# Kernel tuning notes

Hardware: AMD Instinct MI355X
Metric: run time of the kernel (lower is better)

The kernel has to match this reference:

```python
import jax, jax.numpy as jnp
import numpy as np

B, P, H, W = 64, 2, 512, 512

def setup_inputs() -> dict:
    key = jax.random.key(0)
    k1, k2 = jax.random.split(key)
    inp = jax.random.normal(k1, (B, P, H, W), dtype=jnp.float32)
    tgt = jax.random.uniform(k2, (B, P, H, W), dtype=jnp.float32)
    return {"input": inp, "target": tgt}


def reference(input, target):
    b, p, h, w = input.shape  # p == 2 required by the original loss
    # DSNT soft-argmax: softmax over flattened heatmap, expectation over grids
    sm = jax.nn.softmax(input.reshape(b, p, h * w), axis=-1).reshape(b, p, h, w)
    x_grid = (jnp.arange(1, w + 1, dtype=input.dtype)) / w  # [W]
    y_grid = (jnp.arange(1, h + 1, dtype=input.dtype)) / h  # [H]
    pred_x = jnp.einsum('bphw,w->bp', sm, x_grid)
    pred_y = jnp.einsum('bphw,h->bp', sm, y_grid)
    # ground-truth argmax coords (detached / non-differentiable)
    am = jnp.argmax(target.reshape(b, p, h * w), axis=-1)  # [B,P]
    true_x = ((am % w).astype(input.dtype) + 1.0) / w
    true_y = ((am // w).astype(input.dtype) + 1.0) / h
    # euclidean distance loss per (sample, point)
    ed = jnp.sqrt((true_x - pred_x) ** 2 + (true_y - pred_y) ** 2)  # [B,P]
    s = jnp.sum(ed)
    # vector between point 0 and point 1 (x, y) per sample
    pred_vec = jnp.stack([pred_x[:, 0] - pred_x[:, 1], pred_y[:, 0] - pred_y[:, 1]], axis=-1)  # [B,2]
    true_vec = jnp.stack([true_x[:, 0] - true_x[:, 1], true_y[:, 0] - true_y[:, 1]], axis=-1)  # [B,2]
    pred_dist = jnp.sqrt(jnp.sum(pred_vec ** 2, axis=-1))  # [B]
    true_dist = jnp.sqrt(jnp.sum(true_vec ** 2, axis=-1))  # [B]
    s = s + jnp.sum(jnp.sqrt((pred_dist - true_dist) ** 2))
    # NOTE: original applies cos() to the cosine similarity (faithful reproduction)
    dot = jnp.sum(pred_vec * true_vec, axis=-1)  # [B]
    cos_distance = 1.0 - jnp.cos(dot / (pred_dist * true_dist))
    s = s + jnp.sum(cos_distance)
    return jnp.reshape(s / b, (1,))
```

## Files before the change

kernel.cpp:

```cpp
#include <hip/hip_runtime.h>
#include <math.h>

#define HH 512
#define WW 512
#define BP 128
#define PLANE (HH * WW)
#define SEG2 32
#define SEG_FLOATS 8192
#define NPART2 (BP * SEG2)


__device__ __forceinline__ void gload_lds16(const float* g, float* l)
{
    __builtin_amdgcn_global_load_lds(
        (const __attribute__((address_space(1))) void*)g,
        (__attribute__((address_space(3))) void*)l, 16, 0, 0);
}

__global__ __launch_bounds__(256, 2) void dsnt_partial(
    const float* __restrict__ inp, const float* __restrict__ tgt,
    float* __restrict__ wsf, int* __restrict__ wsi)
{
    const int tid  = threadIdx.x;
    const int blk  = blockIdx.x;
    const int lane = tid & 63, wid = tid >> 6;
    const float inv = 1.0f / 512.0f;

    __shared__ float lds[SEG_FLOATS];

    const bool is_sm = (blk < NPART2);
    const int  b2    = is_sm ? blk : blk - NPART2;
    const int  pair  = b2 >> 5;
    const int  seg   = b2 & 31;
    const float* __restrict__ gbase =
        (is_sm ? inp : tgt) + (size_t)pair * PLANE + seg * SEG_FLOATS;
    const int segbase = seg * SEG_FLOATS;

#pragma unroll
    for (int r = 0; r < 8; ++r) {
        const int k = wid * 8 + r;
        gload_lds16(gbase + k * 256 + lane * 4, &lds[k * 256]);
    }
    __syncthreads();

    const float4* __restrict__ lp = (const float4*)lds;

    if (is_sm) {
        float s = 0.0f, sx = 0.0f, sy = 0.0f;
#pragma unroll
        for (int j = 0; j < 8; ++j) {
            const float4 v = lp[j * 256 + tid];
            const int f = segbase + (j * 256 + tid) * 4;
            const float yw  = (float)((f >> 9) + 1) * inv;
            const float xw0 = (float)((f & 511) + 1) * inv;
            const float e0 = __expf(v.x);
            const float e1 = __expf(v.y);
            const float e2 = __expf(v.z);
            const float e3 = __expf(v.w);
            const float es = e0 + e1 + e2 + e3;
            s  += es;
            sx += es * xw0 + inv * (e1 + 2.0f * e2 + 3.0f * e3);
            sy += es * yw;
        }

#pragma unroll
        for (int off = 32; off > 0; off >>= 1) {
            s  += __shfl_down(s,  off, 64);
            sx += __shfl_down(sx, off, 64);
            sy += __shfl_down(sy, off, 64);
        }
        __syncthreads();
        if (lane == 0) { lds[wid] = s; lds[4 + wid] = sx; lds[8 + wid] = sy; }
        __syncthreads();
        if (tid == 0) {
            float fs = lds[0], fsx = lds[4], fsy = lds[8];
#pragma unroll
            for (int k = 1; k < 4; ++k) {
                fs += lds[k]; fsx += lds[4 + k]; fsy += lds[8 + k];
            }
            wsf[blk]              = fs;
            wsf[NPART2 + blk]     = fsx;
            wsf[2 * NPART2 + blk] = fsy;
        }
    } else {
        float mv = -1.0f;
        int   mi = 0;
#pragma unroll
        for (int j = 0; j < 8; ++j) {
            const float4 v = lp[j * 256 + tid];
            const int f = segbase + (j * 256 + tid) * 4;
            if (v.x > mv) { mv = v.x; mi = f; }
            if (v.y > mv) { mv = v.y; mi = f + 1; }
            if (v.z > mv) { mv = v.z; mi = f + 2; }
            if (v.w > mv) { mv = v.w; mi = f + 3; }
        }

#pragma unroll
        for (int off = 32; off > 0; off >>= 1) {
            const float ov = __shfl_down(mv, off, 64);
            const int   oi = __shfl_down(mi, off, 64);
            if (ov > mv || (ov == mv && oi < mi)) { mv = ov; mi = oi; }
        }
        __syncthreads();
        int* ldsi = (int*)lds;
        if (lane == 0) { lds[wid] = mv; ldsi[4 + wid] = mi; }
        __syncthreads();
        if (tid == 0) {
            float fmv = lds[0];
            int   fmi = ldsi[4];
#pragma unroll
            for (int k = 1; k < 4; ++k)
                if (lds[k] > fmv || (lds[k] == fmv && ldsi[4 + k] < fmi)) {
                    fmv = lds[k]; fmi = ldsi[4 + k];
                }
            wsf[3 * NPART2 + b2] = fmv;
            wsi[b2]              = fmi;
        }
    }
}

__global__ __launch_bounds__(128) void dsnt_finalize(
    const float* __restrict__ wsf, const int* __restrict__ wsi,
    float* __restrict__ out)
{
    __shared__ float px[BP], py[BP], tx[BP], ty[BP];
    __shared__ float wsum[2];
    const int tid = threadIdx.x;

    {
        float s = 0.0f, sx = 0.0f, sy = 0.0f, mv = -1.0f;
        int mi = 0;
#pragma unroll
        for (int k = 0; k < SEG2; ++k) {
            const int i = tid * SEG2 + k;
            s  += wsf[i];
            sx += wsf[NPART2 + i];
            sy += wsf[2 * NPART2 + i];
            const float v = wsf[3 * NPART2 + i];
            const int  ii = wsi[i];
            if (v > mv || (v == mv && ii < mi)) { mv = v; mi = ii; }
        }
        px[tid] = sx / s;
        py[tid] = sy / s;
        tx[tid] = (float)((mi & 511) + 1) * (1.0f / 512.0f);
        ty[tid] = (float)((mi >> 9) + 1) * (1.0f / 512.0f);
    }
    __syncthreads();

    float term = 0.0f;
    if (tid < 64) {
        const int b = tid;
        const float px0 = px[2 * b], px1 = px[2 * b + 1];
        const float py0 = py[2 * b], py1 = py[2 * b + 1];
        const float tx0 = tx[2 * b], tx1 = tx[2 * b + 1];
        const float ty0 = ty[2 * b], ty1 = ty[2 * b + 1];

        const float ed0 = sqrtf((tx0 - px0) * (tx0 - px0) + (ty0 - py0) * (ty0 - py0));
        const float ed1 = sqrtf((tx1 - px1) * (tx1 - px1) + (ty1 - py1) * (ty1 - py1));

        const float pvx = px0 - px1, pvy = py0 - py1;
        const float tvx = tx0 - tx1, tvy = ty0 - ty1;
        const float pd = sqrtf(pvx * pvx + pvy * pvy);
        const float td = sqrtf(tvx * tvx + tvy * tvy);
        const float dot = pvx * tvx + pvy * tvy;
        const float cosd = 1.0f - cosf(dot / (pd * td));
        term = ed0 + ed1 + fabsf(pd - td) + cosd;
    }

#pragma unroll
    for (int off = 32; off > 0; off >>= 1)
        term += __shfl_down(term, off, 64);
    const int lane = tid & 63, wid = tid >> 6;
    if (lane == 0) wsum[wid] = term;
    __syncthreads();
    if (tid == 0) out[0] = (wsum[0] + wsum[1]) * (1.0f / 64.0f);
}

extern "C" void kernel_launch(void* const* d_in, const int* in_sizes, int n_in,
                              void* d_out, int out_size, void* d_ws, size_t ws_size,
                              hipStream_t stream)
{
    const float* inp = (const float*)d_in[0];
    const float* tgt = (const float*)d_in[1];
    float* out = (float*)d_out;
    float* wsf = (float*)d_ws;
    int*   wsi = (int*)((float*)d_ws + 4 * NPART2);

    dsnt_partial<<<2 * NPART2, 256, 0, stream>>>(inp, tgt, wsf, wsi);
    dsnt_finalize<<<1, 128, 0, stream>>>(wsf, wsi, out);
}
```

Baseline: 280.6 us.

## Give each wave its own segment with double-buffered async LDS loads

Each wavefront now handles a whole 8192-float segment on its own, so a block covers four segments and the grid shrinks by four. Within a wave, the segment is streamed in 1024-float chunks through two LDS buffers. Direct-to-LDS global loads are issued two chunks ahead and gated with explicit vmcnt/lgkmcnt waits, and the block-level syncthreads and cross-wave LDS reduction are removed. This aims to overlap memory latency with compute and cut barrier overhead. The cost is reliance on hand-written waitcnt counts being correct for the compiler's instruction ordering, plus fewer blocks in flight.

```diff
diff --git a/kernel.cpp b/kernel.cpp
--- a/kernel.cpp
+++ b/kernel.cpp
@@ -8,6 +8,8 @@
 #define SEG2 32
 #define SEG_FLOATS 8192
 #define NPART2 (BP * SEG2)
+#define CHUNK_F 1024
+#define NCHUNK 8
 
 
 __device__ __forceinline__ void gload_lds16(const float* g, float* l)
@@ -17,50 +19,68 @@
         (__attribute__((address_space(3))) void*)l, 16, 0, 0);
 }
 
-__global__ __launch_bounds__(256, 2) void dsnt_partial(
+__device__ __forceinline__ void issue_chunk(const float* gsrc, float* ldst,
+                                            int lane)
+{
+#pragma unroll
+    for (int ld = 0; ld < 4; ++ld)
+        gload_lds16(gsrc + ld * 256 + lane * 4, ldst + ld * 256);
+}
+
+__global__ __launch_bounds__(256) void dsnt_partial(
     const float* __restrict__ inp, const float* __restrict__ tgt,
     float* __restrict__ wsf, int* __restrict__ wsi)
 {
     const int tid  = threadIdx.x;
-    const int blk  = blockIdx.x;
     const int lane = tid & 63, wid = tid >> 6;
     const float inv = 1.0f / 512.0f;
 
-    __shared__ float lds[SEG_FLOATS];
-
-    const bool is_sm = (blk < NPART2);
-    const int  b2    = is_sm ? blk : blk - NPART2;
+    __shared__ float lds[4][2][CHUNK_F];
+
+    const int  g     = blockIdx.x * 4 + wid;
+    const bool is_sm = (g < NPART2);
+    const int  b2    = is_sm ? g : g - NPART2;
     const int  pair  = b2 >> 5;
     const int  seg   = b2 & 31;
     const float* __restrict__ gbase =
         (is_sm ? inp : tgt) + (size_t)pair * PLANE + seg * SEG_FLOATS;
     const int segbase = seg * SEG_FLOATS;
 
-#pragma unroll
-    for (int r = 0; r < 8; ++r) {
-        const int k = wid * 8 + r;
-        gload_lds16(gbase + k * 256 + lane * 4, &lds[k * 256]);
-    }
-    __syncthreads();
-
-    const float4* __restrict__ lp = (const float4*)lds;
+    float* const bufA = &lds[wid][0][0];
+    float* const bufB = &lds[wid][1][0];
+
+    issue_chunk(gbase + 0 * CHUNK_F, bufA, lane);
+    issue_chunk(gbase + 1 * CHUNK_F, bufB, lane);
 
     if (is_sm) {
         float s = 0.0f, sx = 0.0f, sy = 0.0f;
 #pragma unroll
-        for (int j = 0; j < 8; ++j) {
-            const float4 v = lp[j * 256 + tid];
-            const int f = segbase + (j * 256 + tid) * 4;
-            const float yw  = (float)((f >> 9) + 1) * inv;
-            const float xw0 = (float)((f & 511) + 1) * inv;
-            const float e0 = __expf(v.x);
-            const float e1 = __expf(v.y);
-            const float e2 = __expf(v.z);
-            const float e3 = __expf(v.w);
-            const float es = e0 + e1 + e2 + e3;
-            s  += es;
-            sx += es * xw0 + inv * (e1 + 2.0f * e2 + 3.0f * e3);
-            sy += es * yw;
+        for (int c = 0; c < NCHUNK; ++c) {
+            float* const buf = (c & 1) ? bufB : bufA;
+            if (c < NCHUNK - 1)
+                asm volatile("s_waitcnt vmcnt(4)" ::: "memory");
+            else
+                asm volatile("s_waitcnt vmcnt(0)" ::: "memory");
+            const float4* const lp = (const float4*)buf;
+#pragma unroll
+            for (int i = 0; i < 4; ++i) {
+                const float4 v = lp[i * 64 + lane];
+                const int f = segbase + c * CHUNK_F + (i * 64 + lane) * 4;
+                const float yw  = (float)((f >> 9) + 1) * inv;
+                const float xw0 = (float)((f & 511) + 1) * inv;
+                const float e0 = __expf(v.x);
+                const float e1 = __expf(v.y);
+                const float e2 = __expf(v.z);
+                const float e3 = __expf(v.w);
+                const float es = e0 + e1 + e2 + e3;
+                s  += es;
+                sx += es * xw0 + inv * (e1 + 2.0f * e2 + 3.0f * e3);
+                sy += es * yw;
+            }
+            if (c + 2 < NCHUNK) {
+                asm volatile("s_waitcnt lgkmcnt(0)" ::: "memory");
+                issue_chunk(gbase + (c + 2) * CHUNK_F, buf, lane);
+            }
         }
 
 #pragma unroll
@@ -69,30 +89,35 @@
             sx += __shfl_down(sx, off, 64);
             sy += __shfl_down(sy, off, 64);
         }
-        __syncthreads();
-        if (lane == 0) { lds[wid] = s; lds[4 + wid] = sx; lds[8 + wid] = sy; }
-        __syncthreads();
-        if (tid == 0) {
-            float fs = lds[0], fsx = lds[4], fsy = lds[8];
-#pragma unroll
-            for (int k = 1; k < 4; ++k) {
-                fs += lds[k]; fsx += lds[4 + k]; fsy += lds[8 + k];
-            }
-            wsf[blk]              = fs;
-            wsf[NPART2 + blk]     = fsx;
-            wsf[2 * NPART2 + blk] = fsy;
+        if (lane == 0) {
+            wsf[g]              = s;
+            wsf[NPART2 + g]     = sx;
+            wsf[2 * NPART2 + g] = sy;
         }
     } else {
         float mv = -1.0f;
         int   mi = 0;
 #pragma unroll
-        for (int j = 0; j < 8; ++j) {
-            const float4 v = lp[j * 256 + tid];
-            const int f = segbase + (j * 256 + tid) * 4;
-            if (v.x > mv) { mv = v.x; mi = f; }
-            if (v.y > mv) { mv = v.y; mi = f + 1; }
-            if (v.z > mv) { mv = v.z; mi = f + 2; }
-            if (v.w > mv) { mv = v.w; mi = f + 3; }
+        for (int c = 0; c < NCHUNK; ++c) {
+            float* const buf = (c & 1) ? bufB : bufA;
+            if (c < NCHUNK - 1)
+                asm volatile("s_waitcnt vmcnt(4)" ::: "memory");
+            else
+                asm volatile("s_waitcnt vmcnt(0)" ::: "memory");
+            const float4* const lp = (const float4*)buf;
+#pragma unroll
+            for (int i = 0; i < 4; ++i) {
+                const float4 v = lp[i * 64 + lane];
+                const int f = segbase + c * CHUNK_F + (i * 64 + lane) * 4;
+                if (v.x > mv) { mv = v.x; mi = f; }
+                if (v.y > mv) { mv = v.y; mi = f + 1; }
+                if (v.z > mv) { mv = v.z; mi = f + 2; }
+                if (v.w > mv) { mv = v.w; mi = f + 3; }
+            }
+            if (c + 2 < NCHUNK) {
+                asm volatile("s_waitcnt lgkmcnt(0)" ::: "memory");
+                issue_chunk(gbase + (c + 2) * CHUNK_F, buf, lane);
+            }
         }
 
 #pragma unroll
@@ -101,20 +126,9 @@
             const int   oi = __shfl_down(mi, off, 64);
             if (ov > mv || (ov == mv && oi < mi)) { mv = ov; mi = oi; }
         }
-        __syncthreads();
-        int* ldsi = (int*)lds;
-        if (lane == 0) { lds[wid] = mv; ldsi[4 + wid] = mi; }
-        __syncthreads();
-        if (tid == 0) {
-            float fmv = lds[0];
-            int   fmi = ldsi[4];
-#pragma unroll
-            for (int k = 1; k < 4; ++k)
-                if (lds[k] > fmv || (lds[k] == fmv && ldsi[4 + k] < fmi)) {
-                    fmv = lds[k]; fmi = ldsi[4 + k];
-                }
-            wsf[3 * NPART2 + b2] = fmv;
-            wsi[b2]              = fmi;
+        if (lane == 0) {
+            wsf[3 * NPART2 + b2] = mv;
+            wsi[b2]              = mi;
         }
     }
 }
@@ -186,6 +200,6 @@
     float* wsf = (float*)d_ws;
     int*   wsi = (int*)((float*)d_ws + 4 * NPART2);
 
-    dsnt_partial<<<2 * NPART2, 256, 0, stream>>>(inp, tgt, wsf, wsi);
+    dsnt_partial<<<2048, 256, 0, stream>>>(inp, tgt, wsf, wsi);
     dsnt_finalize<<<1, 128, 0, stream>>>(wsf, wsi, out);
 }
```

Result: no change. 281.4 us (+0.3%).
